# Optimization experiments

Measured on AMD Instinct MI355X. Metric: run time of the kernel, lower is better.

## Reference

```python
import jax, jax.numpy as jnp
import numpy as np

ALPHA = 0.2          # LeakyReLU negative slope (args.alpha)
NEG_INF = -9e15      # zero_vec constant from the torch source


def _build_mask(neighbors):
    """Faithful port of A_creat: scatter-add edge counts, row-normalize,
    add self-loops (identity), row-normalize again. neighbors: [N, deg] int."""
    N, deg = neighbors.shape
    rows = jnp.repeat(jnp.arange(N), deg)
    counts = jnp.zeros((N, N), jnp.float32).at[rows, neighbors.reshape(-1)].add(1.0)
    m = counts / counts.sum(axis=1, keepdims=True)
    m = m + jnp.eye(N, dtype=jnp.float32)
    m = m / m.sum(axis=1, keepdims=True)
    return m


def setup_inputs() -> dict:
    key = jax.random.key(0)
    k1, k2, k3, k4 = jax.random.split(key, 4)
    N, F_IN, F_OUT, DEG = 8192, 256, 128, 32
    h = jax.random.normal(k1, (N, F_IN), dtype=jnp.float32)
    neighbors = jax.random.randint(k2, (N, DEG), 0, N)
    # torch uses nn.init.uniform_ (U[0,1)) for both W and a
    W = jax.random.uniform(k3, (F_IN, F_OUT), dtype=jnp.float32)
    a = jax.random.uniform(k4, (2 * F_OUT, 1), dtype=jnp.float32)
    return {"h": h, "W": W, "a": a, "neighbors": neighbors}


def reference(h, W, a, neighbors):
    F_out = W.shape[1]
    mask = _build_mask(neighbors)                 # [N, N]
    hW = h @ W                                    # [N, F_out]
    h1 = hW @ a[:F_out]                           # [N, 1]
    h2 = hW @ a[F_out:]                           # [N, 1]
    e = mask * (h1 + h2.T)                        # dense masked additive scores
    e = jnp.where(e > 0, e, ALPHA * e)            # LeakyReLU
    att = jnp.where(e != 0.0, e, NEG_INF)         # mask out zeros
    att = jax.nn.softmax(att, axis=1)             # row softmax (dropout off in eval)
    feat = att @ hW                               # aggregate
    return jax.nn.elu(feat)
```

## Files before the change

kernel.cpp:

```cpp
#include <hip/hip_runtime.h>
#include <math.h>

#define N_NODES 8192
#define F_IN    256
#define F_OUT   128
#define DEG     32
#define ALPHA   0.2f

__global__ void gemm_hw_kernel(const float* __restrict__ h,
                               const float* __restrict__ W,
                               float* __restrict__ hW) {
    __shared__ float hs[8 * F_IN];
    const int tid  = threadIdx.x;
    const int row0 = blockIdx.x * 8;

    const float4* hsrc = (const float4*)(h + (size_t)row0 * F_IN);
    float4* hdst = (float4*)hs;
    #pragma unroll
    for (int t = 0; t < 4; ++t)
        hdst[tid + t * 128] = hsrc[tid + t * 128];
    __syncthreads();

    float acc[8] = {0.f, 0.f, 0.f, 0.f, 0.f, 0.f, 0.f, 0.f};
    #pragma unroll 4
    for (int k = 0; k < F_IN; ++k) {
        float w = W[k * F_OUT + tid];
        #pragma unroll
        for (int r = 0; r < 8; ++r)
            acc[r] = fmaf(hs[r * F_IN + k], w, acc[r]);
    }
    #pragma unroll
    for (int r = 0; r < 8; ++r)
        hW[(size_t)(row0 + r) * F_OUT + tid] = acc[r];
}

__global__ void h1h2_kernel(const float* __restrict__ hW,
                            const float* __restrict__ a,
                            float* __restrict__ h1,
                            float* __restrict__ h2) {
    const int wave = threadIdx.x >> 6;
    const int lane = threadIdx.x & 63;
    const int row  = blockIdx.x * 4 + wave;
    const float* hr = hW + (size_t)row * F_OUT;

    float s1 = 0.f, s2 = 0.f;
    #pragma unroll
    for (int j = lane; j < F_OUT; j += 64) {
        float v = hr[j];
        s1 = fmaf(v, a[j], s1);
        s2 = fmaf(v, a[F_OUT + j], s2);
    }
    #pragma unroll
    for (int off = 32; off > 0; off >>= 1) {
        s1 += __shfl_down(s1, off);
        s2 += __shfl_down(s2, off);
    }
    if (lane == 0) { h1[row] = s1; h2[row] = s2; }
}

__global__ void attn_kernel(const float* __restrict__ hW,
                            const float* __restrict__ h1,
                            const float* __restrict__ h2,
                            const int*   __restrict__ nbr,
                            float* __restrict__ out) {
    const int wave = threadIdx.x >> 6;
    const int lane = threadIdx.x & 63;
    const int row  = blockIdx.x * 4 + wave;

    int col = -1;
    if (lane < DEG)       col = nbr[(size_t)row * DEG + lane];
    else if (lane == DEG) col = row;

    int cnt = 0;
    int firstq = lane;
    #pragma unroll
    for (int q = 0; q <= DEG; ++q) {
        int cq = __shfl(col, q);
        bool same = (cq == col);
        if (same && q < DEG)    cnt++;
        if (same && q < firstq) firstq = q;
    }
    const bool active = (lane <= DEG) && (col >= 0) && (firstq == lane);

    float mask_val = (float)cnt * (1.0f / 64.0f) + ((col == row) ? 0.5f : 0.0f);

    const float h1row = h1[row];
    float h2c = active ? h2[col] : 0.f;
    float s = mask_val * (h1row + h2c);
    float e = (s > 0.f) ? s : ALPHA * s;
    bool valid = active && (e != 0.0f);

    float ev = valid ? e : -INFINITY;
    #pragma unroll
    for (int off = 32; off > 0; off >>= 1)
        ev = fmaxf(ev, __shfl_xor(ev, off));
    float w = valid ? expf(e - ev) : 0.f;
    float denom = w;
    #pragma unroll
    for (int off = 32; off > 0; off >>= 1)
        denom += __shfl_xor(denom, off);
    float att = w / denom;

    float acc0 = 0.f, acc1 = 0.f;
    #pragma unroll
    for (int q = 0; q <= DEG; ++q) {
        float aq = __shfl(att, q);
        int   cq = __shfl(col, q);
        if (aq > 0.f) {
            const float* hr = hW + (size_t)cq * F_OUT;
            acc0 = fmaf(aq, hr[lane],      acc0);
            acc1 = fmaf(aq, hr[64 + lane], acc1);
        }
    }

    float o0 = (acc0 > 0.f) ? acc0 : expm1f(acc0);
    float o1 = (acc1 > 0.f) ? acc1 : expm1f(acc1);
    out[(size_t)row * F_OUT + lane]      = o0;
    out[(size_t)row * F_OUT + 64 + lane] = o1;
}

extern "C" void kernel_launch(void* const* d_in, const int* in_sizes, int n_in,
                              void* d_out, int out_size, void* d_ws, size_t ws_size,
                              hipStream_t stream) {
    const float* h   = (const float*)d_in[0];
    const float* W   = (const float*)d_in[1];
    const float* a   = (const float*)d_in[2];
    const int*   nbr = (const int*)  d_in[3];
    float* out = (float*)d_out;

    float* hW = (float*)d_ws;
    float* h1 = hW + (size_t)N_NODES * F_OUT;
    float* h2 = h1 + N_NODES;

    gemm_hw_kernel<<<N_NODES / 8, 128, 0, stream>>>(h, W, hW);
    h1h2_kernel   <<<N_NODES / 4, 256, 0, stream>>>(hW, a, h1, h2);
    attn_kernel   <<<N_NODES / 4, 256, 0, stream>>>(hW, h1, h2, nbr, out);
}
```

Baseline: 102.8 us.

## Register-tile the hW GEMM, fuse h1/h2 projections, vectorize attention gathers

The GEMM is rewritten as a 32-row block tile with 4x4 register micro-tiles, LDS-staged h and W chunks, and register prefetch of the next K chunk. The h1/h2 dot products are fused into the GEMM epilogue, which removes one kernel launch and a re-read of hW. In the attention kernel, each lane now owns two adjacent columns, so gathers and stores use float2. The exact exp and expm1 calls are swapped for __expf, which costs some accuracy near zero in the ELU.

```diff
diff --git a/kernel.cpp b/kernel.cpp
--- a/kernel.cpp
+++ b/kernel.cpp
@@ -7,62 +7,139 @@
 #define DEG     32
 #define ALPHA   0.2f
 
-__global__ void gemm_hw_kernel(const float* __restrict__ h,
-                               const float* __restrict__ W,
-                               float* __restrict__ hW) {
-    __shared__ float hs[8 * F_IN];
+#define MT      32
+#define KC      64
+#define HPAD    68
+
+__global__ __launch_bounds__(256) void gemm_fused_kernel(
+        const float* __restrict__ h,
+        const float* __restrict__ W,
+        const float* __restrict__ a,
+        float* __restrict__ hW,
+        float* __restrict__ h1,
+        float* __restrict__ h2) {
+    __shared__ float h_tile[MT * HPAD];
+    __shared__ float W_tile[KC * F_OUT];
+
     const int tid  = threadIdx.x;
-    const int row0 = blockIdx.x * 8;
-
-    const float4* hsrc = (const float4*)(h + (size_t)row0 * F_IN);
-    float4* hdst = (float4*)hs;
-    #pragma unroll
-    for (int t = 0; t < 4; ++t)
-        hdst[tid + t * 128] = hsrc[tid + t * 128];
+    const int row0 = blockIdx.x * MT;
+    const int c0   = (tid & 31) * 4;
+    const int r0   = (tid >> 5) * 4;
+
+    float acc[4][4];
+    #pragma unroll
+    for (int i = 0; i < 4; ++i)
+        #pragma unroll
+        for (int j = 0; j < 4; ++j) acc[i][j] = 0.f;
+
+    float4 hbuf[2], wbuf[8];
+    auto issue_loads = [&](int kc) {
+        #pragma unroll
+        for (int p = 0; p < 2; ++p) {
+            int lin = tid + p * 256;
+            int r   = lin >> 4;
+            int kq  = (lin & 15) * 4;
+            hbuf[p] = *(const float4*)(h + (size_t)(row0 + r) * F_IN + kc + kq);
+        }
+        #pragma unroll
+        for (int p = 0; p < 8; ++p) {
+            int lin = tid + p * 256;
+            int kr  = lin >> 5;
+            int cq  = (lin & 31) * 4;
+            wbuf[p] = *(const float4*)(W + (size_t)(kc + kr) * F_OUT + cq);
+        }
+    };
+    auto commit_lds = [&]() {
+        #pragma unroll
+        for (int p = 0; p < 2; ++p) {
+            int lin = tid + p * 256;
+            int r   = lin >> 4;
+            int kq  = (lin & 15) * 4;
+            *(float4*)(h_tile + r * HPAD + kq) = hbuf[p];
+        }
+        #pragma unroll
+        for (int p = 0; p < 8; ++p) {
+            int lin = tid + p * 256;
+            int kr  = lin >> 5;
+            int cq  = (lin & 31) * 4;
+            *(float4*)(W_tile + kr * F_OUT + cq) = wbuf[p];
+        }
+    };
+
+    issue_loads(0);
+    commit_lds();
     __syncthreads();
 
-    float acc[8] = {0.f, 0.f, 0.f, 0.f, 0.f, 0.f, 0.f, 0.f};
-    #pragma unroll 4
-    for (int k = 0; k < F_IN; ++k) {
-        float w = W[k * F_OUT + tid];
-        #pragma unroll
-        for (int r = 0; r < 8; ++r)
-            acc[r] = fmaf(hs[r * F_IN + k], w, acc[r]);
-    }
-    #pragma unroll
-    for (int r = 0; r < 8; ++r)
-        hW[(size_t)(row0 + r) * F_OUT + tid] = acc[r];
+    #pragma unroll
+    for (int ch = 0; ch < F_IN / KC; ++ch) {
+        if (ch + 1 < F_IN / KC) issue_loads((ch + 1) * KC);
+
+        #pragma unroll
+        for (int k4 = 0; k4 < KC; k4 += 4) {
+            float4 hv[4], wv[4];
+            #pragma unroll
+            for (int i = 0; i < 4; ++i)
+                hv[i] = *(const float4*)(h_tile + (r0 + i) * HPAD + k4);
+            #pragma unroll
+            for (int kk = 0; kk < 4; ++kk)
+                wv[kk] = *(const float4*)(W_tile + (k4 + kk) * F_OUT + c0);
+            #pragma unroll
+            for (int i = 0; i < 4; ++i) {
+                const float hv0[4] = {hv[i].x, hv[i].y, hv[i].z, hv[i].w};
+                #pragma unroll
+                for (int kk = 0; kk < 4; ++kk) {
+                    acc[i][0] = fmaf(hv0[kk], wv[kk].x, acc[i][0]);
+                    acc[i][1] = fmaf(hv0[kk], wv[kk].y, acc[i][1]);
+                    acc[i][2] = fmaf(hv0[kk], wv[kk].z, acc[i][2]);
+                    acc[i][3] = fmaf(hv0[kk], wv[kk].w, acc[i][3]);
+                }
+            }
+        }
+        __syncthreads();
+        if (ch + 1 < F_IN / KC) {
+            commit_lds();
+            __syncthreads();
+        }
+    }
+
+    #pragma unroll
+    for (int i = 0; i < 4; ++i) {
+        float4 v = make_float4(acc[i][0], acc[i][1], acc[i][2], acc[i][3]);
+        *(float4*)(hW + (size_t)(row0 + r0 + i) * F_OUT + c0) = v;
+    }
+
+    float a1v[4], a2v[4];
+    #pragma unroll
+    for (int j = 0; j < 4; ++j) {
+        a1v[j] = a[c0 + j];
+        a2v[j] = a[F_OUT + c0 + j];
+    }
+    #pragma unroll
+    for (int i = 0; i < 4; ++i) {
+        float s1 = 0.f, s2 = 0.f;
+        #pragma unroll
+        for (int j = 0; j < 4; ++j) {
+            s1 = fmaf(acc[i][j], a1v[j], s1);
+            s2 = fmaf(acc[i][j], a2v[j], s2);
+        }
+        #pragma unroll
+        for (int off = 1; off < 32; off <<= 1) {
+            s1 += __shfl_xor(s1, off);
+            s2 += __shfl_xor(s2, off);
+        }
+        if ((tid & 31) == 0) {
+            h1[row0 + r0 + i] = s1;
+            h2[row0 + r0 + i] = s2;
+        }
+    }
 }
 
-__global__ void h1h2_kernel(const float* __restrict__ hW,
-                            const float* __restrict__ a,
-                            float* __restrict__ h1,
-                            float* __restrict__ h2) {
-    const int wave = threadIdx.x >> 6;
-    const int lane = threadIdx.x & 63;
-    const int row  = blockIdx.x * 4 + wave;
-    const float* hr = hW + (size_t)row * F_OUT;
-
-    float s1 = 0.f, s2 = 0.f;
-    #pragma unroll
-    for (int j = lane; j < F_OUT; j += 64) {
-        float v = hr[j];
-        s1 = fmaf(v, a[j], s1);
-        s2 = fmaf(v, a[F_OUT + j], s2);
-    }
-    #pragma unroll
-    for (int off = 32; off > 0; off >>= 1) {
-        s1 += __shfl_down(s1, off);
-        s2 += __shfl_down(s2, off);
-    }
-    if (lane == 0) { h1[row] = s1; h2[row] = s2; }
-}
-
-__global__ void attn_kernel(const float* __restrict__ hW,
-                            const float* __restrict__ h1,
-                            const float* __restrict__ h2,
-                            const int*   __restrict__ nbr,
-                            float* __restrict__ out) {
+__global__ __launch_bounds__(256) void attn_kernel(
+        const float* __restrict__ hW,
+        const float* __restrict__ h1,
+        const float* __restrict__ h2,
+        const int*   __restrict__ nbr,
+        float* __restrict__ out) {
     const int wave = threadIdx.x >> 6;
     const int lane = threadIdx.x & 63;
     const int row  = blockIdx.x * 4 + wave;
@@ -94,7 +171,7 @@
     #pragma unroll
     for (int off = 32; off > 0; off >>= 1)
         ev = fmaxf(ev, __shfl_xor(ev, off));
-    float w = valid ? expf(e - ev) : 0.f;
+    float w = valid ? __expf(e - ev) : 0.f;
     float denom = w;
     #pragma unroll
     for (int off = 32; off > 0; off >>= 1)
@@ -107,16 +184,15 @@
         float aq = __shfl(att, q);
         int   cq = __shfl(col, q);
         if (aq > 0.f) {
-            const float* hr = hW + (size_t)cq * F_OUT;
-            acc0 = fmaf(aq, hr[lane],      acc0);
-            acc1 = fmaf(aq, hr[64 + lane], acc1);
-        }
-    }
-
-    float o0 = (acc0 > 0.f) ? acc0 : expm1f(acc0);
-    float o1 = (acc1 > 0.f) ? acc1 : expm1f(acc1);
-    out[(size_t)row * F_OUT + lane]      = o0;
-    out[(size_t)row * F_OUT + 64 + lane] = o1;
+            float2 v = *(const float2*)(hW + (size_t)cq * F_OUT + 2 * lane);
+            acc0 = fmaf(aq, v.x, acc0);
+            acc1 = fmaf(aq, v.y, acc1);
+        }
+    }
+
+    float o0 = (acc0 > 0.f) ? acc0 : (__expf(acc0) - 1.0f);
+    float o1 = (acc1 > 0.f) ? acc1 : (__expf(acc1) - 1.0f);
+    *(float2*)(out + (size_t)row * F_OUT + 2 * lane) = make_float2(o0, o1);
 }
 
 extern "C" void kernel_launch(void* const* d_in, const int* in_sizes, int n_in,
@@ -132,7 +208,6 @@
     float* h1 = hW + (size_t)N_NODES * F_OUT;
     float* h2 = h1 + N_NODES;
 
-    gemm_hw_kernel<<<N_NODES / 8, 128, 0, stream>>>(h, W, hW);
-    h1h2_kernel   <<<N_NODES / 4, 256, 0, stream>>>(hW, a, h1, h2);
-    attn_kernel   <<<N_NODES / 4, 256, 0, stream>>>(hW, h1, h2, nbr, out);
+    gemm_fused_kernel<<<N_NODES / MT, 256, 0, stream>>>(h, W, a, hW, h1, h2);
+    attn_kernel      <<<N_NODES / 4,  256, 0, stream>>>(hW, h1, h2, nbr, out);
 }
```

Result: slower. 113.7 us (+10.6%).

## Use bf16 MFMA for hW GEMM, fold attention vectors into W, store hW in bf16

Applied to the files above, without the earlier changes.

Replaces the scalar fp32 h@W kernel with a bf16 MFMA 16x16x32 kernel, using a small pre-pass that packs W into the MFMA fragment layout. h1/h2 are computed as h·(W a) from precomputed W·a vectors inside the GEMM, which removes the separate h1h2 pass. hW is stored in bf16 to halve the gather traffic in the attention kernel, which also switches to fast exp and vectorized stores. This trades accuracy (bf16 inputs and an intermediate rounded to bf16) for less compute time and memory traffic.

```diff
diff --git a/kernel.cpp b/kernel.cpp
--- a/kernel.cpp
+++ b/kernel.cpp
@@ -7,62 +7,131 @@
 #define DEG     32
 #define ALPHA   0.2f
 
-__global__ void gemm_hw_kernel(const float* __restrict__ h,
-                               const float* __restrict__ W,
-                               float* __restrict__ hW) {
-    __shared__ float hs[8 * F_IN];
+typedef __attribute__((ext_vector_type(8))) short short8;
+typedef __attribute__((ext_vector_type(4))) float floatx4;
+
+__device__ __forceinline__ unsigned short f2bf(float x) {
+    unsigned u = __float_as_uint(x);
+    return (unsigned short)((u + 0x7fffu + ((u >> 16) & 1u)) >> 16);
+}
+
+__global__ __launch_bounds__(64) void pack_w_kernel(
+        const float* __restrict__ W, unsigned short* __restrict__ Wtf) {
+    const int lane = threadIdx.x;
+    const int quad = lane >> 4;
+    const int l15  = lane & 15;
+    const int kt   = blockIdx.x >> 3;
+    const int gnt  = blockIdx.x & 7;
+    const int n    = gnt * 16 + l15;
+    const int kb   = kt * 32 + quad * 8;
+
+    unsigned short s[8];
+    #pragma unroll
+    for (int j = 0; j < 8; ++j)
+        s[j] = f2bf(W[(size_t)(kb + j) * F_OUT + n]);
+
+    uint4 p;
+    p.x = (unsigned)s[0] | ((unsigned)s[1] << 16);
+    p.y = (unsigned)s[2] | ((unsigned)s[3] << 16);
+    p.z = (unsigned)s[4] | ((unsigned)s[5] << 16);
+    p.w = (unsigned)s[6] | ((unsigned)s[7] << 16);
+    ((uint4*)Wtf)[(size_t)blockIdx.x * 64 + lane] = p;
+}
+
+__global__ __launch_bounds__(64) void wa_kernel(
+        const float* __restrict__ W, const float* __restrict__ a,
+        float* __restrict__ wa1, float* __restrict__ wa2) {
+    const int k = blockIdx.x * 64 + threadIdx.x;
+    const float* wr = W + (size_t)k * F_OUT;
+    float s1 = 0.f, s2 = 0.f;
+    #pragma unroll 4
+    for (int n = 0; n < F_OUT; n += 4) {
+        float4 wv = *(const float4*)(wr + n);
+        float4 a1 = *(const float4*)(a + n);
+        float4 a2 = *(const float4*)(a + F_OUT + n);
+        s1 = fmaf(wv.x, a1.x, fmaf(wv.y, a1.y, fmaf(wv.z, a1.z, fmaf(wv.w, a1.w, s1))));
+        s2 = fmaf(wv.x, a2.x, fmaf(wv.y, a2.y, fmaf(wv.z, a2.z, fmaf(wv.w, a2.w, s2))));
+    }
+    wa1[k] = s1;
+    wa2[k] = s2;
+}
+
+__global__ __launch_bounds__(256) void gemm_mfma_v6(
+        const float* __restrict__ h,
+        const unsigned short* __restrict__ Wtf,
+        const float* __restrict__ wa1,
+        const float* __restrict__ wa2,
+        unsigned short* __restrict__ hWb,
+        float* __restrict__ h1,
+        float* __restrict__ h2) {
     const int tid  = threadIdx.x;
-    const int row0 = blockIdx.x * 8;
-
-    const float4* hsrc = (const float4*)(h + (size_t)row0 * F_IN);
-    float4* hdst = (float4*)hs;
-    #pragma unroll
-    for (int t = 0; t < 4; ++t)
-        hdst[tid + t * 128] = hsrc[tid + t * 128];
-    __syncthreads();
-
-    float acc[8] = {0.f, 0.f, 0.f, 0.f, 0.f, 0.f, 0.f, 0.f};
-    #pragma unroll 4
-    for (int k = 0; k < F_IN; ++k) {
-        float w = W[k * F_OUT + tid];
+    const int wave = tid >> 6;
+    const int lane = tid & 63;
+    const int quad = lane >> 4;
+    const int l15  = lane & 15;
+    const int row0 = blockIdx.x * 16;
+
+    const float* hrow = h + (size_t)(row0 + l15) * F_IN + quad * 8;
+    const short8* Wf  = (const short8*)Wtf;
+
+    floatx4 acc[2] = {{0.f,0.f,0.f,0.f},{0.f,0.f,0.f,0.f}};
+    float s1 = 0.f, s2 = 0.f;
+
+    #pragma unroll
+    for (int kt = 0; kt < 8; ++kt) {
+        float4 v0 = *(const float4*)(hrow + kt * 32);
+        float4 v1 = *(const float4*)(hrow + kt * 32 + 4);
+        short8 af;
+        af[0] = (short)f2bf(v0.x); af[1] = (short)f2bf(v0.y);
+        af[2] = (short)f2bf(v0.z); af[3] = (short)f2bf(v0.w);
+        af[4] = (short)f2bf(v1.x); af[5] = (short)f2bf(v1.y);
+        af[6] = (short)f2bf(v1.z); af[7] = (short)f2bf(v1.w);
+
         #pragma unroll
-        for (int r = 0; r < 8; ++r)
-            acc[r] = fmaf(hs[r * F_IN + k], w, acc[r]);
-    }
-    #pragma unroll
-    for (int r = 0; r < 8; ++r)
-        hW[(size_t)(row0 + r) * F_OUT + tid] = acc[r];
-}
-
-__global__ void h1h2_kernel(const float* __restrict__ hW,
-                            const float* __restrict__ a,
-                            float* __restrict__ h1,
-                            float* __restrict__ h2) {
-    const int wave = threadIdx.x >> 6;
-    const int lane = threadIdx.x & 63;
-    const int row  = blockIdx.x * 4 + wave;
-    const float* hr = hW + (size_t)row * F_OUT;
-
-    float s1 = 0.f, s2 = 0.f;
-    #pragma unroll
-    for (int j = lane; j < F_OUT; j += 64) {
-        float v = hr[j];
-        s1 = fmaf(v, a[j], s1);
-        s2 = fmaf(v, a[F_OUT + j], s2);
-    }
-    #pragma unroll
-    for (int off = 32; off > 0; off >>= 1) {
-        s1 += __shfl_down(s1, off);
-        s2 += __shfl_down(s2, off);
-    }
-    if (lane == 0) { h1[row] = s1; h2[row] = s2; }
-}
-
-__global__ void attn_kernel(const float* __restrict__ hW,
-                            const float* __restrict__ h1,
-                            const float* __restrict__ h2,
-                            const int*   __restrict__ nbr,
-                            float* __restrict__ out) {
+        for (int nt = 0; nt < 2; ++nt) {
+            short8 bf = Wf[(size_t)(kt * 8 + wave * 2 + nt) * 64 + lane];
+            acc[nt] = __builtin_amdgcn_mfma_f32_16x16x32_bf16(af, bf, acc[nt], 0, 0, 0);
+        }
+
+        if (wave == 0) {
+            const int kb = kt * 32 + quad * 8;
+            float4 u0 = *(const float4*)(wa1 + kb);
+            float4 u1 = *(const float4*)(wa1 + kb + 4);
+            float4 t0 = *(const float4*)(wa2 + kb);
+            float4 t1 = *(const float4*)(wa2 + kb + 4);
+            s1 = fmaf(v0.x,u0.x, fmaf(v0.y,u0.y, fmaf(v0.z,u0.z, fmaf(v0.w,u0.w, s1))));
+            s1 = fmaf(v1.x,u1.x, fmaf(v1.y,u1.y, fmaf(v1.z,u1.z, fmaf(v1.w,u1.w, s1))));
+            s2 = fmaf(v0.x,t0.x, fmaf(v0.y,t0.y, fmaf(v0.z,t0.z, fmaf(v0.w,t0.w, s2))));
+            s2 = fmaf(v1.x,t1.x, fmaf(v1.y,t1.y, fmaf(v1.z,t1.z, fmaf(v1.w,t1.w, s2))));
+        }
+    }
+
+    #pragma unroll
+    for (int nt = 0; nt < 2; ++nt) {
+        const int col = wave * 32 + nt * 16 + l15;
+        #pragma unroll
+        for (int reg = 0; reg < 4; ++reg) {
+            const int row = row0 + quad * 4 + reg;
+            hWb[(size_t)row * F_OUT + col] = f2bf(acc[nt][reg]);
+        }
+    }
+
+    if (wave == 0) {
+        s1 += __shfl_xor(s1, 16); s1 += __shfl_xor(s1, 32);
+        s2 += __shfl_xor(s2, 16); s2 += __shfl_xor(s2, 32);
+        if (lane < 16) {
+            h1[row0 + l15] = s1;
+            h2[row0 + l15] = s2;
+        }
+    }
+}
+
+__global__ __launch_bounds__(256) void attn_kernel(
+        const unsigned int* __restrict__ hWb,
+        const float* __restrict__ h1,
+        const float* __restrict__ h2,
+        const int*   __restrict__ nbr,
+        float* __restrict__ out) {
     const int wave = threadIdx.x >> 6;
     const int lane = threadIdx.x & 63;
     const int row  = blockIdx.x * 4 + wave;
@@ -94,7 +163,7 @@
     #pragma unroll
     for (int off = 32; off > 0; off >>= 1)
         ev = fmaxf(ev, __shfl_xor(ev, off));
-    float w = valid ? expf(e - ev) : 0.f;
+    float w = valid ? __expf(e - ev) : 0.f;
     float denom = w;
     #pragma unroll
     for (int off = 32; off > 0; off >>= 1)
@@ -107,16 +176,17 @@
         float aq = __shfl(att, q);
         int   cq = __shfl(col, q);
         if (aq > 0.f) {
-            const float* hr = hW + (size_t)cq * F_OUT;
-            acc0 = fmaf(aq, hr[lane],      acc0);
-            acc1 = fmaf(aq, hr[64 + lane], acc1);
+            unsigned v = hWb[(size_t)cq * (F_OUT / 2) + lane];
+            float lo = __uint_as_float(v << 16);
+            float hi = __uint_as_float(v & 0xffff0000u);
+            acc0 = fmaf(aq, lo, acc0);
+            acc1 = fmaf(aq, hi, acc1);
         }
     }
 
     float o0 = (acc0 > 0.f) ? acc0 : expm1f(acc0);
     float o1 = (acc1 > 0.f) ? acc1 : expm1f(acc1);
-    out[(size_t)row * F_OUT + lane]      = o0;
-    out[(size_t)row * F_OUT + 64 + lane] = o1;
+    *(float2*)(out + (size_t)row * F_OUT + 2 * lane) = make_float2(o0, o1);
 }
 
 extern "C" void kernel_launch(void* const* d_in, const int* in_sizes, int n_in,
@@ -128,11 +198,16 @@
     const int*   nbr = (const int*)  d_in[3];
     float* out = (float*)d_out;
 
-    float* hW = (float*)d_ws;
-    float* h1 = hW + (size_t)N_NODES * F_OUT;
+    unsigned short* hWb = (unsigned short*)d_ws;
+    float* h1 = (float*)(hWb + (size_t)N_NODES * F_OUT);
     float* h2 = h1 + N_NODES;
-
-    gemm_hw_kernel<<<N_NODES / 8, 128, 0, stream>>>(h, W, hW);
-    h1h2_kernel   <<<N_NODES / 4, 256, 0, stream>>>(hW, a, h1, h2);
-    attn_kernel   <<<N_NODES / 4, 256, 0, stream>>>(hW, h1, h2, nbr, out);
-}
+    unsigned short* Wtf = (unsigned short*)(h2 + N_NODES);
+    float* wa1 = (float*)(Wtf + (size_t)F_IN * F_OUT);
+    float* wa2 = wa1 + F_IN;
+
+    pack_w_kernel<<<64, 64, 0, stream>>>(W, Wtf);
+    wa_kernel    <<<4,  64, 0, stream>>>(W, a, wa1, wa2);
+    gemm_mfma_v6 <<<N_NODES / 16, 256, 0, stream>>>(h, Wtf, wa1, wa2, hWb, h1, h2);
+    attn_kernel  <<<N_NODES / 4,  256, 0, stream>>>((const unsigned int*)hWb,
+                                                    h1, h2, nbr, out);
+}
```

Measured after the change: 94.04 us. 8.5% less time.
